# Kernel tuning notes

Hardware: AMD Instinct MI355X
Metric: run time of the kernel (lower is better)

Reference implementation:

```python
import jax, jax.numpy as jnp
import numpy as np

N, E, D, L, G = 50000, 1600000, 128, 3, 64


def setup_inputs() -> dict:
    key = jax.random.key(0)
    ks = jax.random.split(key, 10)
    s = 1.0 / np.sqrt(D).astype(np.float32)
    X = jax.random.normal(ks[0], (N, D), jnp.float32)
    edge_index = jax.random.randint(ks[1], (2, E), 0, N, dtype=jnp.int32)
    edge_types = jax.random.randint(ks[2], (E,), 0, 2, dtype=jnp.int32)
    batch_ids = jnp.sort(jax.random.randint(ks[3], (N,), 0, G, dtype=jnp.int32))
    Wd = jax.random.uniform(ks[4], (L, D, D), jnp.float32, -s, s)
    bd = jax.random.uniform(ks[5], (L, D), jnp.float32, -s, s)
    Wc = jax.random.uniform(ks[6], (L, D, D), jnp.float32, -s, s)
    bc = jax.random.uniform(ks[7], (L, D), jnp.float32, -s, s)
    Ws = jax.random.uniform(ks[8], (L, D, D), jnp.float32, -s, s)
    bs = jax.random.uniform(ks[9], (L, D), jnp.float32, -s, s)
    return dict(X=X, Wd=Wd, bd=bd, Wc=Wc, bc=bc, Ws=Ws, bs=bs,
                edge_index=edge_index, edge_types=edge_types, batch_ids=batch_ids)


def reference(X, Wd, bd, Wc, bc, Ws, bs, edge_index, edge_types, batch_ids):
    src, dst = edge_index[0], edge_index[1]
    is_data = (edge_types == 0)[:, None]  # [E,1] edge-type selector
    for l in range(L):
        # Linear commutes with gather: compute node-level GEMMs once,
        # then per-edge gather + type select (same math as per-edge Linear).
        Xd = X @ Wd[l] + bd[l]            # [N,D] data-edge messages
        Xc = X @ Wc[l] + bc[l]            # [N,D] control-edge messages
        msg = jnp.where(is_data, Xd[src], Xc[src])      # [E,D]
        agg = jax.ops.segment_sum(msg, dst, num_segments=N)  # scatter-add
        X = jax.nn.relu(agg + X @ Ws[l] + bs[l])
    # global mean pool per graph
    sums = jax.ops.segment_sum(X, batch_ids, num_segments=G)
    cnts = jax.ops.segment_sum(jnp.ones((N,), X.dtype), batch_ids, num_segments=G)
    return sums / jnp.maximum(cnts, 1.0)[:, None]
```

## Files before the change

### kernel.cpp

```cpp
#include <hip/hip_runtime.h>
#include <hip/hip_fp16.h>

#define N_NODES 50000
#define N_EDGES 1600000
#define DIM     128
#define NLAYERS 3
#define NGRAPHS 64

#define NBUCK   196
#define CSR_BLKS 256
#define EPB     (N_EDGES / CSR_BLKS)
#define EITER   ((EPB + 255) / 256)

typedef _Float16 half8 __attribute__((ext_vector_type(8)));
typedef float    f32x4 __attribute__((ext_vector_type(4)));
typedef float    f32x2 __attribute__((ext_vector_type(2)));

#define LDK 136

__device__ __forceinline__ unsigned char f32_to_fp8(float v) {
    int q = __builtin_amdgcn_cvt_pk_fp8_f32(v, v, 0, false);
    return (unsigned char)(q & 0xFF);
}

__global__ __launch_bounds__(256) void setup_kernel(
        const float* __restrict__ X, __half* __restrict__ Xh,
        unsigned char* __restrict__ X8,
        const float* __restrict__ Wd, const float* __restrict__ Wc,
        const float* __restrict__ Ws, __half* __restrict__ WT,
        float* __restrict__ sums, int* __restrict__ gcnt) {
    int i = blockIdx.x * 256 + threadIdx.x;
    if (i < N_NODES * DIM / 4) {
        float4 v = *(const float4*)(X + (size_t)i * 4);
        union { __half2 h2[2]; uint2 u; } pk;
        pk.h2[0] = __floats2half2_rn(v.x, v.y);
        pk.h2[1] = __floats2half2_rn(v.z, v.w);
        *(uint2*)(Xh + (size_t)i * 4) = pk.u;
        int q0 = __builtin_amdgcn_cvt_pk_fp8_f32(v.x, v.y, 0, false);
        int q1 = __builtin_amdgcn_cvt_pk_fp8_f32(v.z, v.w, q0, true);
        *(unsigned int*)(X8 + (size_t)i * 4) = (unsigned int)q1;
    }
    if (i < 9 * DIM * DIM) {
        int k  = i & 127;
        int n  = (i >> 7) & 127;
        int lw = i >> 14;
        int l  = lw / 3, w = lw - 3 * l;
        const float* W = ((w == 0) ? Wd : (w == 1) ? Wc : Ws)
                         + (size_t)l * DIM * DIM;
        WT[i] = __float2half(W[k * DIM + n]);
    }
    if (i < NGRAPHS * DIM) sums[i] = 0.f;
    if (i < NGRAPHS) gcnt[i] = 0;
}

__global__ __launch_bounds__(256) void csr1_kernel(const int* __restrict__ dst,
                                                   int* __restrict__ cntmat) {
    __shared__ int hc[NBUCK];
    int tid = threadIdx.x;
    for (int i = tid; i < NBUCK; i += 256) hc[i] = 0;
    __syncthreads();
    int base = blockIdx.x * EPB;
#pragma unroll
    for (int i = 0; i < EITER; ++i) {
        int idx = i * 256 + tid;
        if (idx < EPB) atomicAdd(&hc[dst[base + idx] >> 8], 1);
    }
    __syncthreads();
    for (int i = tid; i < NBUCK; i += 256)
        cntmat[i * CSR_BLKS + blockIdx.x] = hc[i];
}

__global__ __launch_bounds__(256) void scanA_kernel(const int* __restrict__ cntmat,
                                                    int* __restrict__ exc,
                                                    int* __restrict__ btot) {
    __shared__ int sh[256];
    int tid = threadIdx.x, b = blockIdx.x;
    int v = cntmat[b * CSR_BLKS + tid];
    sh[tid] = v;
    __syncthreads();
    for (int o = 1; o < 256; o <<= 1) {
        int t = (tid >= o) ? sh[tid - o] : 0;
        __syncthreads();
        sh[tid] += t;
        __syncthreads();
    }
    exc[b * CSR_BLKS + tid] = sh[tid] - v;
    if (tid == 255) btot[b] = sh[255];
}

__global__ __launch_bounds__(256) void csr2_kernel(const int* __restrict__ src,
                                                   const int* __restrict__ dst,
                                                   const int* __restrict__ et,
                                                   const int* __restrict__ exc,
                                                   const int* __restrict__ btot,
                                                   int* __restrict__ bstart,
                                                   int* __restrict__ esv) {
    __shared__ int sh[256];
    __shared__ int bst[NBUCK];
    __shared__ int cur[NBUCK];
    int tid = threadIdx.x;
    int v = (tid < NBUCK) ? btot[tid] : 0;
    sh[tid] = v;
    __syncthreads();
    for (int o = 1; o < 256; o <<= 1) {
        int t = (tid >= o) ? sh[tid - o] : 0;
        __syncthreads();
        sh[tid] += t;
        __syncthreads();
    }
    if (tid < NBUCK) bst[tid] = sh[tid] - v;
    if (blockIdx.x == 0) {
        if (tid < NBUCK) bstart[tid] = sh[tid] - v;
        if (tid == NBUCK - 1) bstart[NBUCK] = sh[tid];
    }
    __syncthreads();
    if (tid < NBUCK) cur[tid] = exc[tid * CSR_BLKS + blockIdx.x] + bst[tid];
    __syncthreads();
    int base = blockIdx.x * EPB;
#pragma unroll
    for (int i = 0; i < EITER; ++i) {
        int idx = i * 256 + tid;
        if (idx < EPB) {
            int e = base + idx;
            int d = dst[e];
            int pos = atomicAdd(&cur[d >> 8], 1);
            esv[pos] = (src[e] + et[e] * N_NODES) | ((d & 255) << 17);
        }
    }
}

__global__ __launch_bounds__(256) void csr3_kernel(const int* __restrict__ esv,
                                                   const int* __restrict__ bstart,
                                                   int* __restrict__ col,
                                                   int* __restrict__ row_start,
                                                   int* __restrict__ deg,
                                                   int* __restrict__ degd) {
    __shared__ int cnt[256];
    __shared__ int cntd[256];
    __shared__ int sh[256];
    __shared__ int curD[256];
    __shared__ int curC[256];
    int tid = threadIdx.x, b = blockIdx.x;
    int bs = bstart[b], be = bstart[b + 1];
    cnt[tid] = 0;
    cntd[tid] = 0;
    __syncthreads();
    for (int e = bs + tid; e < be; e += 256) {
        int pk = esv[e];
        int nd = (pk >> 17) & 255;
        atomicAdd(&cnt[nd], 1);
        if ((pk & 0x1FFFF) < N_NODES) atomicAdd(&cntd[nd], 1);
    }
    __syncthreads();
    int v = cnt[tid];
    sh[tid] = v;
    __syncthreads();
    for (int o = 1; o < 256; o <<= 1) {
        int t = (tid >= o) ? sh[tid - o] : 0;
        __syncthreads();
        sh[tid] += t;
        __syncthreads();
    }
    int off  = sh[tid] - v;
    int node = (b << 8) + tid;
    if (node < N_NODES) {
        row_start[node] = bs + off;
        deg[node]       = v;
        degd[node]      = cntd[tid];
    }
    curD[tid] = bs + off;
    curC[tid] = bs + off + cntd[tid];
    __syncthreads();
    for (int e = bs + tid; e < be; e += 256) {
        int pk  = esv[e];
        int nd  = (pk >> 17) & 255;
        int sv  = pk & 0x1FFFF;
        int isC = sv >= N_NODES;
        int pos = atomicAdd(isC ? &curC[nd] : &curD[nd], 1);
        col[pos] = sv - (isC ? N_NODES : 0);
    }
}

__device__ __forceinline__ void agg_range(
        const int* __restrict__ col, const unsigned char* __restrict__ X8,
        unsigned off, int base, int cnt, float* a) {
    if (cnt <= 0) return;
    int last = cnt - 1;
    int nb = (cnt + 7) >> 3;
    int p[8];
#pragma unroll
    for (int i = 0; i < 8; ++i)
        p[i] = col[base + (i < cnt ? i : last)];
    for (int b = 0; b < nb; ++b) {
        int e0 = b * 8;
        uint2 v[8];
#pragma unroll
        for (int i = 0; i < 8; ++i)
            v[i] = *(const uint2*)(X8 + (((unsigned)p[i] << 7) | off));
        int pn[8];
        if (b + 1 < nb) {
            int e1 = e0 + 8;
#pragma unroll
            for (int i = 0; i < 8; ++i) {
                int idx = e1 + i;
                pn[i] = col[base + (idx < cnt ? idx : last)];
            }
        }
#pragma unroll
        for (int i = 0; i < 8; ++i)
            if (e0 + i >= cnt) { v[i].x = 0u; v[i].y = 0u; }
#pragma unroll
        for (int i = 0; i < 8; ++i) {
            f32x2 f0 = __builtin_amdgcn_cvt_pk_f32_fp8(v[i].x, false);
            f32x2 f1 = __builtin_amdgcn_cvt_pk_f32_fp8(v[i].x, true);
            f32x2 f2 = __builtin_amdgcn_cvt_pk_f32_fp8(v[i].y, false);
            f32x2 f3 = __builtin_amdgcn_cvt_pk_f32_fp8(v[i].y, true);
            a[0] += f0[0]; a[1] += f0[1];
            a[2] += f1[0]; a[3] += f1[1];
            a[4] += f2[0]; a[5] += f2[1];
            a[6] += f3[0]; a[7] += f3[1];
        }
        if (b + 1 < nb) {
#pragma unroll
            for (int i = 0; i < 8; ++i) p[i] = pn[i];
        }
    }
}

__global__ __launch_bounds__(256) void agg_kernel(
        const int* __restrict__ row_start, const int* __restrict__ deg_arr,
        const int* __restrict__ degd_arr, const int* __restrict__ col,
        const unsigned char* __restrict__ X8,
        __half* __restrict__ Sd, __half* __restrict__ Sc) {
    int wave = (blockIdx.x * 256 + threadIdx.x) >> 6;
    int lane = threadIdx.x & 63;
    int grp  = lane >> 4;
    int l16  = lane & 15;
    int node = wave * 4 + grp;
    if (node >= N_NODES) return;

    int rs = row_start[node];
    int dg = deg_arr[node];
    int dd = degd_arr[node];
    const unsigned off = (unsigned)l16 * 8;

    float aD[8], aC[8];
#pragma unroll
    for (int j = 0; j < 8; ++j) { aD[j] = 0.f; aC[j] = 0.f; }

    agg_range(col, X8, off, rs, dd, aD);
    agg_range(col, X8, off, rs + dd, dg - dd, aC);

    union { __half2 h2[4]; uint4 u; } pd, pc;
#pragma unroll
    for (int j = 0; j < 4; ++j) {
        pd.h2[j] = __floats2half2_rn(aD[2 * j], aD[2 * j + 1]);
        pc.h2[j] = __floats2half2_rn(aC[2 * j], aC[2 * j + 1]);
    }
    *(uint4*)(Sd + (size_t)node * DIM + off) = pd.u;
    *(uint4*)(Sc + (size_t)node * DIM + off) = pc.u;
}

__global__ __launch_bounds__(256) void gemm_fused_kernel(
        const __half* __restrict__ Sd, const __half* __restrict__ Sc,
        const __half* __restrict__ Xh,
        const __half* __restrict__ WTl,
        const float* __restrict__ bd, const float* __restrict__ bc,
        const float* __restrict__ bs,
        const int* __restrict__ degd, const int* __restrict__ deg,
        __half* __restrict__ Xh_out, unsigned char* __restrict__ X8_out,
        int write8) {
    __shared__ _Float16 As[64 * LDK];
    __shared__ _Float16 Bs[128 * LDK];

    const int tid = threadIdx.x;
    const int m0  = blockIdx.x * 64;

    const int wv = tid >> 6;
    const int l  = tid & 63;
    const int lm = l & 15;
    const int q  = l >> 4;

    f32x4 acc[4][2];
#pragma unroll
    for (int mt = 0; mt < 4; ++mt) {
        acc[mt][0] = (f32x4){0.f, 0.f, 0.f, 0.f};
        acc[mt][1] = (f32x4){0.f, 0.f, 0.f, 0.f};
    }

    for (int w = 0; w < 3; ++w) {
        if (w) __syncthreads();
        const __half* Asrc = (w == 0) ? Sd : (w == 1) ? Sc : Xh;
#pragma unroll
        for (int i = 0; i < 4; ++i) {
            int c    = i * 256 + tid;
            int row  = c >> 4;
            int colh = (c & 15) * 8;
            uint4 v  = make_uint4(0u, 0u, 0u, 0u);
            int gr   = m0 + row;
            if (gr < N_NODES) v = *(const uint4*)(Asrc + (size_t)gr * DIM + colh);
            *(uint4*)(As + row * LDK + colh) = v;
        }
        {
            const __half* Wt = WTl + (size_t)w * DIM * DIM;
#pragma unroll
            for (int i = 0; i < 8; ++i) {
                int c    = i * 256 + tid;
                int row  = c >> 4;
                int colh = (c & 15) * 8;
                uint4 v = *(const uint4*)(Wt + (size_t)row * DIM + colh);
                *(uint4*)(Bs + row * LDK + colh) = v;
            }
        }
        __syncthreads();

#pragma unroll
        for (int ks = 0; ks < 4; ++ks) {
            int coff = ks * 32 + q * 8;
            half8 am[4];
#pragma unroll
            for (int mt = 0; mt < 4; ++mt)
                am[mt] = *(const half8*)(As + (mt * 16 + lm) * LDK + coff);
            half8 bb0 = *(const half8*)(Bs + (wv * 32 + lm) * LDK + coff);
            half8 bb1 = *(const half8*)(Bs + (wv * 32 + 16 + lm) * LDK + coff);
#pragma unroll
            for (int mt = 0; mt < 4; ++mt) {
                acc[mt][0] = __builtin_amdgcn_mfma_f32_16x16x32_f16(bb0, am[mt], acc[mt][0], 0, 0, 0);
                acc[mt][1] = __builtin_amdgcn_mfma_f32_16x16x32_f16(bb1, am[mt], acc[mt][1], 0, 0, 0);
            }
        }
    }

    const int fb0 = wv * 32 + q * 4;
    const int fb1 = fb0 + 16;
    f32x4 bdv0 = *(const f32x4*)(bd + fb0), bdv1 = *(const f32x4*)(bd + fb1);
    f32x4 bcv0 = *(const f32x4*)(bc + fb0), bcv1 = *(const f32x4*)(bc + fb1);
    f32x4 bsv0 = *(const f32x4*)(bs + fb0), bsv1 = *(const f32x4*)(bs + fb1);
#pragma unroll
    for (int mt = 0; mt < 4; ++mt) {
        int row = m0 + mt * 16 + lm;
        if (row < N_NODES) {
            float dd = (float)degd[row];
            float dc = (float)(deg[row] - degd[row]);
            float v0[4], v1[4];
#pragma unroll
            for (int r = 0; r < 4; ++r) {
                v0[r] = fmaxf(acc[mt][0][r] + dd * bdv0[r] + dc * bcv0[r] + bsv0[r], 0.f);
                v1[r] = fmaxf(acc[mt][1][r] + dd * bdv1[r] + dc * bcv1[r] + bsv1[r], 0.f);
            }
            union { __half2 h2[2]; uint2 u; } p0, p1;
            p0.h2[0] = __floats2half2_rn(v0[0], v0[1]);
            p0.h2[1] = __floats2half2_rn(v0[2], v0[3]);
            p1.h2[0] = __floats2half2_rn(v1[0], v1[1]);
            p1.h2[1] = __floats2half2_rn(v1[2], v1[3]);
            *(uint2*)(Xh_out + (size_t)row * DIM + fb0) = p0.u;
            *(uint2*)(Xh_out + (size_t)row * DIM + fb1) = p1.u;
            if (write8) {
                int q0 = __builtin_amdgcn_cvt_pk_fp8_f32(v0[0], v0[1], 0, false);
                q0 = __builtin_amdgcn_cvt_pk_fp8_f32(v0[2], v0[3], q0, true);
                int q1 = __builtin_amdgcn_cvt_pk_fp8_f32(v1[0], v1[1], 0, false);
                q1 = __builtin_amdgcn_cvt_pk_fp8_f32(v1[2], v1[3], q1, true);
                *(unsigned int*)(X8_out + (size_t)row * DIM + fb0) = (unsigned)q0;
                *(unsigned int*)(X8_out + (size_t)row * DIM + fb1) = (unsigned)q1;
            }
        }
    }
}

__global__ __launch_bounds__(256) void pool_kernel(const __half* __restrict__ X,
                                                   const int* __restrict__ bid,
                                                   float* __restrict__ sums,
                                                   int* __restrict__ gcnt) {
    __shared__ float acc[8][DIM];
    __shared__ int scnt[8];
    __shared__ int sgmin;
    int tid = threadIdx.x;
    for (int i = tid; i < 8 * DIM; i += 256) ((float*)acc)[i] = 0.f;
    if (tid < 8) scnt[tid] = 0;
    int n0 = blockIdx.x * 64;
    if (tid == 0) sgmin = bid[n0];
    __syncthreads();
    int gmin = sgmin;

    int s    = tid >> 5;
    int lane = tid & 31;
    int r0   = n0 + s * 8;

    int g[8];
    union { uint2 u; __half2 h2[2]; } v[8];
#pragma unroll
    for (int i = 0; i < 8; ++i) {
        int r = r0 + i;
        g[i] = (r < N_NODES) ? bid[r] : -1;
    }
#pragma unroll
    for (int i = 0; i < 8; ++i) {
        int r = r0 + i;
        if (r < N_NODES)
            v[i].u = *(const uint2*)(X + (size_t)r * DIM + lane * 4);
        else { v[i].u.x = 0u; v[i].u.y = 0u; }
    }

    float4 a = make_float4(0.f, 0.f, 0.f, 0.f);
    int cur = -1, run = 0;
#pragma unroll
    for (int i = 0; i < 8; ++i) {
        if (g[i] != cur) {
            if (cur >= 0) {
                int slot = cur - gmin;
                if (slot < 8) {
                    atomicAdd(&acc[slot][lane * 4 + 0], a.x);
                    atomicAdd(&acc[slot][lane * 4 + 1], a.y);
                    atomicAdd(&acc[slot][lane * 4 + 2], a.z);
                    atomicAdd(&acc[slot][lane * 4 + 3], a.w);
                    if (lane == 0) atomicAdd(&scnt[slot], run);
                } else {
                    atomicAdd(&sums[cur * DIM + lane * 4 + 0], a.x);
                    atomicAdd(&sums[cur * DIM + lane * 4 + 1], a.y);
                    atomicAdd(&sums[cur * DIM + lane * 4 + 2], a.z);
                    atomicAdd(&sums[cur * DIM + lane * 4 + 3], a.w);
                    if (lane == 0) atomicAdd(&gcnt[cur], run);
                }
            }
            cur = g[i];
            a = make_float4(0.f, 0.f, 0.f, 0.f);
            run = 0;
        }
        if (g[i] >= 0) {
            float2 f0 = __half22float2(v[i].h2[0]);
            float2 f1 = __half22float2(v[i].h2[1]);
            a.x += f0.x; a.y += f0.y; a.z += f1.x; a.w += f1.y;
            run++;
        }
    }
    if (cur >= 0) {
        int slot = cur - gmin;
        if (slot < 8) {
            atomicAdd(&acc[slot][lane * 4 + 0], a.x);
            atomicAdd(&acc[slot][lane * 4 + 1], a.y);
            atomicAdd(&acc[slot][lane * 4 + 2], a.z);
            atomicAdd(&acc[slot][lane * 4 + 3], a.w);
            if (lane == 0) atomicAdd(&scnt[slot], run);
        } else {
            atomicAdd(&sums[cur * DIM + lane * 4 + 0], a.x);
            atomicAdd(&sums[cur * DIM + lane * 4 + 1], a.y);
            atomicAdd(&sums[cur * DIM + lane * 4 + 2], a.z);
            atomicAdd(&sums[cur * DIM + lane * 4 + 3], a.w);
            if (lane == 0) atomicAdd(&gcnt[cur], run);
        }
    }
    __syncthreads();

    for (int slot = 0; slot < 8; ++slot) {
        if (scnt[slot] > 0) {
            int gg = gmin + slot;
            for (int i = tid; i < DIM; i += 256)
                atomicAdd(&sums[gg * DIM + i], acc[slot][i]);
            if (tid == 0) atomicAdd(&gcnt[gg], scnt[slot]);
        }
    }
}

__global__ __launch_bounds__(256) void div_kernel(const float* __restrict__ sums,
                                                  const int* __restrict__ gcnt,
                                                  float* __restrict__ out) {
    int i = blockIdx.x * 256 + threadIdx.x;
    if (i < NGRAPHS * DIM) {
        int g = i >> 7;
        out[i] = sums[i] / fmaxf((float)gcnt[g], 1.f);
    }
}

extern "C" void kernel_launch(void* const* d_in, const int* in_sizes, int n_in,
                              void* d_out, int out_size, void* d_ws, size_t ws_size,
                              hipStream_t stream) {
    const float* Xin = (const float*)d_in[0];
    const float* Wd  = (const float*)d_in[1];
    const float* bd  = (const float*)d_in[2];
    const float* Wc  = (const float*)d_in[3];
    const float* bc  = (const float*)d_in[4];
    const float* Ws  = (const float*)d_in[5];
    const float* bs  = (const float*)d_in[6];
    const int* edge_index = (const int*)d_in[7];
    const int* edge_types = (const int*)d_in[8];
    const int* batch_ids  = (const int*)d_in[9];

    const int* src = edge_index;
    const int* dst = edge_index + N_EDGES;

    const size_t NBH = (size_t)N_NODES * DIM * sizeof(__half);
    const size_t NB8 = (size_t)N_NODES * DIM;
    char* w = (char*)d_ws;
    auto take = [&](size_t bytes) {
        char* p = w;
        w += (bytes + 255) & ~(size_t)255;
        return p;
    };
    __half* Xh0  = (__half*)take(NBH);
    __half* Xh1  = (__half*)take(NBH);
    unsigned char* X8a = (unsigned char*)take(NB8);
    unsigned char* X8b = (unsigned char*)take(NB8);
    __half* SdB  = (__half*)take(NBH);
    __half* ScB  = (__half*)take(NBH);
    __half* WT   = (__half*)take((size_t)9 * DIM * DIM * sizeof(__half));
    int* col     = (int*)take((size_t)N_EDGES * 4);
    int* esv     = (int*)take((size_t)N_EDGES * 4);
    int* cntmat  = (int*)take((size_t)NBUCK * CSR_BLKS * 4);
    int* exc     = (int*)take((size_t)NBUCK * CSR_BLKS * 4);
    int* btot    = (int*)take((size_t)NBUCK * 4);
    int* bstart  = (int*)take((size_t)(NBUCK + 1) * 4);
    int* rowst   = (int*)take((size_t)N_NODES * 4);
    int* deg     = (int*)take((size_t)N_NODES * 4);
    int* degd    = (int*)take((size_t)N_NODES * 4);
    float* sums  = (float*)take((size_t)NGRAPHS * DIM * 4);
    int* gcnt    = (int*)take(NGRAPHS * 4);

    setup_kernel<<<(N_NODES * DIM / 4 + 255) / 256, 256, 0, stream>>>(
        Xin, Xh0, X8a, Wd, Wc, Ws, WT, sums, gcnt);

    csr1_kernel<<<CSR_BLKS, 256, 0, stream>>>(dst, cntmat);
    scanA_kernel<<<NBUCK, 256, 0, stream>>>(cntmat, exc, btot);
    csr2_kernel<<<CSR_BLKS, 256, 0, stream>>>(src, dst, edge_types, exc,
                                              btot, bstart, esv);
    csr3_kernel<<<NBUCK, 256, 0, stream>>>(esv, bstart, col, rowst, deg, degd);

    const int GEMM_MBLK = (N_NODES + 63) / 64;
    const int AGG_BLKS  = (N_NODES + 15) / 16;

    const __half*      Xhc = Xh0;
    const unsigned char* X8c = X8a;
    __half*            XhN[3] = {Xh1, Xh0, Xh1};
    unsigned char*     X8N[3] = {X8b, X8a, X8b};
    for (int l = 0; l < NLAYERS; ++l) {
        agg_kernel<<<AGG_BLKS, 256, 0, stream>>>(rowst, deg, degd, col, X8c,
                                                 SdB, ScB);
        gemm_fused_kernel<<<GEMM_MBLK, 256, 0, stream>>>(
            SdB, ScB, Xhc, WT + (size_t)l * 3 * DIM * DIM,
            bd + (size_t)l * DIM, bc + (size_t)l * DIM, bs + (size_t)l * DIM,
            degd, deg, XhN[l], X8N[l], (l < NLAYERS - 1) ? 1 : 0);
        Xhc = XhN[l];
        X8c = X8N[l];
    }

    const int POOL_BLKS = (N_NODES + 63) / 64;
    pool_kernel<<<POOL_BLKS, 256, 0, stream>>>(Xhc, batch_ids, sums, gcnt);
    div_kernel<<<(NGRAPHS * DIM + 255) / 256, 256, 0, stream>>>(sums, gcnt,
                                                                (float*)d_out);
}
```

Measured before the change: 314.3 us.

## Slice fp8 node features into 32-byte column slices and use 16-bit CSR indices

The fp8 feature copy is stored as four column slices of 32 bytes per node. Setup and the GEMM epilogue write into this layout, and the aggregation kernel gives each block one slice for 64 nodes, with 4 lanes per node. CSR column indices shrink from 32-bit to 16-bit, which works because node ids are below 65536. The aim is a smaller gather working set per slice for better cache reuse and less index traffic, but each edge list is now read four times and each gather request is narrower.

```diff
diff --git a/kernel.cpp b/kernel.cpp
--- a/kernel.cpp
+++ b/kernel.cpp
@@ -12,16 +12,15 @@
 #define EPB     (N_EDGES / CSR_BLKS)
 #define EITER   ((EPB + 255) / 256)
 
+#define NSLICE  4
+#define SLB     32
+#define SLICE_BYTES ((size_t)N_NODES * SLB)
+
 typedef _Float16 half8 __attribute__((ext_vector_type(8)));
 typedef float    f32x4 __attribute__((ext_vector_type(4)));
 typedef float    f32x2 __attribute__((ext_vector_type(2)));
 
 #define LDK 136
-
-__device__ __forceinline__ unsigned char f32_to_fp8(float v) {
-    int q = __builtin_amdgcn_cvt_pk_fp8_f32(v, v, 0, false);
-    return (unsigned char)(q & 0xFF);
-}
 
 __global__ __launch_bounds__(256) void setup_kernel(
         const float* __restrict__ X, __half* __restrict__ Xh,
@@ -38,7 +37,12 @@
         *(uint2*)(Xh + (size_t)i * 4) = pk.u;
         int q0 = __builtin_amdgcn_cvt_pk_fp8_f32(v.x, v.y, 0, false);
         int q1 = __builtin_amdgcn_cvt_pk_fp8_f32(v.z, v.w, q0, true);
-        *(unsigned int*)(X8 + (size_t)i * 4) = (unsigned int)q1;
+        int n  = i >> 5;
+        int j0 = (i & 31) * 4;
+        int sl = j0 >> 5;
+        int sb = j0 & 31;
+        *(unsigned int*)(X8 + sl * SLICE_BYTES + (size_t)n * SLB + sb) =
+            (unsigned int)q1;
     }
     if (i < 9 * DIM * DIM) {
         int k  = i & 127;
@@ -131,7 +135,7 @@
 
 __global__ __launch_bounds__(256) void csr3_kernel(const int* __restrict__ esv,
                                                    const int* __restrict__ bstart,
-                                                   int* __restrict__ col,
+                                                   unsigned short* __restrict__ col,
                                                    int* __restrict__ row_start,
                                                    int* __restrict__ deg,
                                                    int* __restrict__ degd) {
@@ -177,12 +181,13 @@
         int sv  = pk & 0x1FFFF;
         int isC = sv >= N_NODES;
         int pos = atomicAdd(isC ? &curC[nd] : &curD[nd], 1);
-        col[pos] = sv - (isC ? N_NODES : 0);
+        col[pos] = (unsigned short)(sv - (isC ? N_NODES : 0));
     }
 }
 
 __device__ __forceinline__ void agg_range(
-        const int* __restrict__ col, const unsigned char* __restrict__ X8,
+        const unsigned short* __restrict__ col,
+        const unsigned char* __restrict__ Xs,
         unsigned off, int base, int cnt, float* a) {
     if (cnt <= 0) return;
     int last = cnt - 1;
@@ -196,7 +201,7 @@
         uint2 v[8];
 #pragma unroll
         for (int i = 0; i < 8; ++i)
-            v[i] = *(const uint2*)(X8 + (((unsigned)p[i] << 7) | off));
+            v[i] = *(const uint2*)(Xs + (((unsigned)p[i] * SLB) | off));
         int pn[8];
         if (b + 1 < nb) {
             int e1 = e0 + 8;
@@ -229,27 +234,31 @@
 
 __global__ __launch_bounds__(256) void agg_kernel(
         const int* __restrict__ row_start, const int* __restrict__ deg_arr,
-        const int* __restrict__ degd_arr, const int* __restrict__ col,
-        const unsigned char* __restrict__ X8,
+        const int* __restrict__ degd_arr,
+        const unsigned short* __restrict__ col,
+        const unsigned char* __restrict__ X8t,
         __half* __restrict__ Sd, __half* __restrict__ Sc) {
-    int wave = (blockIdx.x * 256 + threadIdx.x) >> 6;
-    int lane = threadIdx.x & 63;
-    int grp  = lane >> 4;
-    int l16  = lane & 15;
-    int node = wave * 4 + grp;
+    int b    = blockIdx.x;
+    int s    = b & (NSLICE - 1);
+    int nb   = b >> 2;
+    int tid  = threadIdx.x;
+    int nl   = tid >> 2;
+    int l4   = tid & 3;
+    int node = nb * 64 + nl;
     if (node >= N_NODES) return;
 
     int rs = row_start[node];
     int dg = deg_arr[node];
     int dd = degd_arr[node];
-    const unsigned off = (unsigned)l16 * 8;
+    const unsigned char* Xs = X8t + (size_t)s * SLICE_BYTES;
+    const unsigned off = (unsigned)l4 * 8;
 
     float aD[8], aC[8];
 #pragma unroll
     for (int j = 0; j < 8; ++j) { aD[j] = 0.f; aC[j] = 0.f; }
 
-    agg_range(col, X8, off, rs, dd, aD);
-    agg_range(col, X8, off, rs + dd, dg - dd, aC);
+    agg_range(col, Xs, off, rs, dd, aD);
+    agg_range(col, Xs, off, rs + dd, dg - dd, aC);
 
     union { __half2 h2[4]; uint4 u; } pd, pc;
 #pragma unroll
@@ -257,8 +266,9 @@
         pd.h2[j] = __floats2half2_rn(aD[2 * j], aD[2 * j + 1]);
         pc.h2[j] = __floats2half2_rn(aC[2 * j], aC[2 * j + 1]);
     }
-    *(uint4*)(Sd + (size_t)node * DIM + off) = pd.u;
-    *(uint4*)(Sc + (size_t)node * DIM + off) = pc.u;
+    size_t so = (size_t)node * DIM + s * SLB + l4 * 8;
+    *(uint4*)(Sd + so) = pd.u;
+    *(uint4*)(Sc + so) = pc.u;
 }
 
 __global__ __launch_bounds__(256) void gemm_fused_kernel(
@@ -360,8 +370,10 @@
                 q0 = __builtin_amdgcn_cvt_pk_fp8_f32(v0[2], v0[3], q0, true);
                 int q1 = __builtin_amdgcn_cvt_pk_fp8_f32(v1[0], v1[1], 0, false);
                 q1 = __builtin_amdgcn_cvt_pk_fp8_f32(v1[2], v1[3], q1, true);
-                *(unsigned int*)(X8_out + (size_t)row * DIM + fb0) = (unsigned)q0;
-                *(unsigned int*)(X8_out + (size_t)row * DIM + fb1) = (unsigned)q1;
+                unsigned char* xb = X8_out + (size_t)wv * SLICE_BYTES
+                                  + (size_t)row * SLB;
+                *(unsigned int*)(xb + q * 4)      = (unsigned)q0;
+                *(unsigned int*)(xb + q * 4 + 16) = (unsigned)q1;
             }
         }
     }
@@ -503,7 +515,7 @@
     __half* SdB  = (__half*)take(NBH);
     __half* ScB  = (__half*)take(NBH);
     __half* WT   = (__half*)take((size_t)9 * DIM * DIM * sizeof(__half));
-    int* col     = (int*)take((size_t)N_EDGES * 4);
+    unsigned short* col = (unsigned short*)take((size_t)N_EDGES * 2);
     int* esv     = (int*)take((size_t)N_EDGES * 4);
     int* cntmat  = (int*)take((size_t)NBUCK * CSR_BLKS * 4);
     int* exc     = (int*)take((size_t)NBUCK * CSR_BLKS * 4);
@@ -525,7 +537,7 @@
     csr3_kernel<<<NBUCK, 256, 0, stream>>>(esv, bstart, col, rowst, deg, degd);
 
     const int GEMM_MBLK = (N_NODES + 63) / 64;
-    const int AGG_BLKS  = (N_NODES + 15) / 16;
+    const int AGG_BLKS  = ((N_NODES + 63) / 64) * NSLICE;
 
     const __half*      Xhc = Xh0;
     const unsigned char* X8c = X8a;
```

Result: slower. 337.6 us (+7.4%).
